# Kernel optimization log

Hardware: AMD Instinct MI355X
Metric: run time of the kernel (lower is better)

The kernel has to match this reference:

```python
import jax, jax.numpy as jnp
import numpy as np

N_NODES = 20000
NC = 16
NUM_BASIS = 5
MAX_CENTER = 3.5

# Real-basis Clebsch-Gordan tensors C[m, m_f, m_o] for the (l, l_f) -> l_o paths.
# Real l=1 basis ordered (m=-1,0,1) = (y,z,x); (y,z,x) is a cyclic permutation of
# (x,y,z) so the standard Levi-Civita gives the 1x1->1 coupling.
_C000 = np.ones((1, 1, 1), dtype=np.float32)
_C011 = np.eye(3, dtype=np.float32).reshape(1, 3, 3)
_C101 = np.eye(3, dtype=np.float32).reshape(3, 1, 3)
_C110 = (np.eye(3, dtype=np.float32) / np.sqrt(3.0)).reshape(3, 3, 1)
_eps = np.zeros((3, 3, 3), dtype=np.float32)
for (i, j, k) in [(0, 1, 2), (1, 2, 0), (2, 0, 1)]:
    _eps[i, j, k] = 1.0
    _eps[i, k, j] = -1.0
_C111 = (_eps / np.sqrt(2.0)).astype(np.float32)

Y00 = 0.28209479177387814  # 1 / (2 sqrt(pi))
Y1C = 0.4886025119029199   # sqrt(3 / (4 pi))


def _spherical_filter(edges, coeffs, l_f):
    """SphericalFilter.__call__: RBF radial part x solid harmonics. -> [E, n_c, 2l_f+1]."""
    centers = jnp.linspace(0.0, MAX_CENTER, NUM_BASIS)
    spread = (MAX_CENTER - 0.0) / NUM_BASIS  # (max - min) / num_basis = 0.7
    radius = jnp.linalg.norm(edges, ord=2, axis=-1)              # [E]
    rbfs = jnp.exp(-spread * (radius[:, None] - centers) ** 2)   # [E, num_basis]
    rad = rbfs @ coeffs.T                                        # [E, n_c]
    if l_f == 0:
        y = jnp.full(edges.shape[:-1] + (1,), Y00, dtype=edges.dtype)
    else:  # l_f == 1: solid harmonics r^1 * Y_1m, order (y, z, x)
        y = Y1C * edges[:, jnp.array([1, 2, 0])]
    y = jnp.nan_to_num(y)
    return rad[:, :, None] * y[:, None, :]


def _tp(nodes, filt, cg, w):
    """Depthwise CG tensor product: [E,c,m],[E,c,f],[m,f,o] -> w[c] * [E,c,o]."""
    out = jnp.einsum('ecm,ecf,mfo->eco', nodes, filt, jnp.asarray(cg))
    return w[None, :, None] * out


def setup_inputs() -> dict:
    key = jax.random.key(0)
    ks = jax.random.split(key, 16)
    E = 640000
    inp = {
        'coords': jax.random.normal(ks[0], (N_NODES, 3), dtype=jnp.float32),
        'nodes0': jax.random.normal(ks[1], (N_NODES, NC, 1), dtype=jnp.float32),
        'nodes1': jax.random.normal(ks[2], (N_NODES, NC, 3), dtype=jnp.float32),
        'edges': jax.random.normal(ks[3], (E, 3), dtype=jnp.float32),
        'senders': jax.random.randint(ks[4], (E,), 0, N_NODES, dtype=jnp.int32),
        'receivers': jax.random.randint(ks[5], (E,), 0, N_NODES, dtype=jnp.int32),
        'coeffs_00': jax.random.uniform(ks[6], (NC, NUM_BASIS), dtype=jnp.float32),
        'coeffs_01': jax.random.uniform(ks[7], (NC, NUM_BASIS), dtype=jnp.float32),
        'coeffs_10': jax.random.uniform(ks[8], (NC, NUM_BASIS), dtype=jnp.float32),
        'coeffs_11': jax.random.uniform(ks[9], (NC, NUM_BASIS), dtype=jnp.float32),
        'w_000': jax.random.normal(ks[10], (NC,), dtype=jnp.float32) + 1.0,
        'w_011': jax.random.normal(ks[11], (NC,), dtype=jnp.float32) + 1.0,
        'w_101': jax.random.normal(ks[12], (NC,), dtype=jnp.float32) + 1.0,
        'w_110': jax.random.normal(ks[13], (NC,), dtype=jnp.float32) + 1.0,
        'w_111': jax.random.normal(ks[14], (NC,), dtype=jnp.float32) + 1.0,
    }
    return inp


def reference(coords, nodes0, nodes1, edges, senders, receivers,
              coeffs_00, coeffs_01, coeffs_10, coeffs_11,
              w_000, w_011, w_101, w_110, w_111):
    # Gather sender node features once per l.
    n0s = nodes0[senders]  # [E, NC, 1]
    n1s = nodes1[senders]  # [E, NC, 3]

    # Filters (loop order: l=0 filters [l_f=0, l_f=1], then l=1 filters).
    f00 = _spherical_filter(edges, coeffs_00, 0)  # [E, NC, 1]
    f01 = _spherical_filter(edges, coeffs_01, 1)  # [E, NC, 3]
    f10 = _spherical_filter(edges, coeffs_10, 0)  # [E, NC, 1]
    f11 = _spherical_filter(edges, coeffs_11, 1)  # [E, NC, 3]

    # Tensor-product messages, concatenated per output degree along channels.
    # l_o = 0 paths: (l=0, l_f=0), (l=1, l_f=1)
    m0 = jnp.concatenate([
        _tp(n0s, f00, _C000, w_000),
        _tp(n1s, f11, _C110, w_110),
    ], axis=-2)  # [E, 2*NC, 1]
    # l_o = 1 paths: (0,1), (1,0), (1,1)
    m1 = jnp.concatenate([
        _tp(n0s, f01, _C011, w_011),
        _tp(n1s, f10, _C101, w_101),
        _tp(n1s, f11, _C111, w_111),
    ], axis=-2)  # [E, 3*NC, 3]

    new0 = jax.ops.segment_sum(m0, receivers, num_segments=N_NODES)
    new1 = jax.ops.segment_sum(m1, receivers, num_segments=N_NODES)
    return coords, new0, new1
```

## Files before the change

kernel.cpp:

```cpp
#include <hip/hip_runtime.h>

#define E_EDGES 640000
#define NN 20000
#define NC 16
#define PBIN 64

#define Y00F 0.28209479177387814f
#define Y1CF 0.4886025119029199f
#define RS3  0.5773502691896258f
#define RS2  0.7071067811865476f

typedef float nf4 __attribute__((ext_vector_type(4)));

struct Acc {
    float a000, a110;
    float a011x, a011y, a011z;
    float a101x, a101y, a101z;
    float a111x, a111y, a111z;
};

__device__ __forceinline__ void edge_body(const nf4 rec,
                                          const float* __restrict__ nodes0,
                                          const float* __restrict__ nodes1,
                                          const float k00[5], const float k01[5],
                                          const float k10[5], const float k11[5],
                                          int c, Acc& A) {
    int s = __float_as_int(rec.w);
    float r = sqrtf(rec.x * rec.x + rec.y * rec.y + rec.z * rec.z);
    float rbf[5];
#pragma unroll
    for (int b = 0; b < 5; b++) {
        float d = r - 0.875f * (float)b;
        rbf[b] = __expf(-0.7f * d * d);
    }
    float rad00 = 0.f, rad01 = 0.f, rad10 = 0.f, rad11 = 0.f;
#pragma unroll
    for (int b = 0; b < 5; b++) {
        rad00 = fmaf(rbf[b], k00[b], rad00);
        rad01 = fmaf(rbf[b], k01[b], rad01);
        rad10 = fmaf(rbf[b], k10[b], rad10);
        rad11 = fmaf(rbf[b], k11[b], rad11);
    }
    float n0 = nodes0[s * NC + c];
    const float* n1p = nodes1 + (s * NC + c) * 3;
    float n1a = n1p[0], n1b = n1p[1], n1c = n1p[2];
    float py = rec.y, pz = rec.z, px = rec.x;
    A.a000 = fmaf(n0, rad00, A.a000);
    A.a110 = fmaf(rad11, n1a * py + n1b * pz + n1c * px, A.a110);
    float kA = n0 * rad01;
    A.a011x = fmaf(kA, py, A.a011x);
    A.a011y = fmaf(kA, pz, A.a011y);
    A.a011z = fmaf(kA, px, A.a011z);
    A.a101x = fmaf(rad10, n1a, A.a101x);
    A.a101y = fmaf(rad10, n1b, A.a101y);
    A.a101z = fmaf(rad10, n1c, A.a101z);
    A.a111x = fmaf(rad11, n1b * px - n1c * pz, A.a111x);
    A.a111y = fmaf(rad11, n1c * py - n1a * px, A.a111y);
    A.a111z = fmaf(rad11, n1a * pz - n1b * py, A.a111z);
}


__global__ void init1_kernel(const float* __restrict__ coords,
                             float* __restrict__ out,
                             int* __restrict__ cnt,
                             int* __restrict__ ovf_count) {
    int i = blockIdx.x * blockDim.x + threadIdx.x;
    if (i < 3 * NN) out[i] = coords[i];
    if (i < NN) cnt[i] = 0;
    if (i == 0) *ovf_count = 0;
}

__global__ void bin_kernel(const float* __restrict__ edges,
                           const int* __restrict__ senders,
                           const int* __restrict__ receivers,
                           int* __restrict__ cnt,
                           nf4* __restrict__ bins,
                           int* __restrict__ ovf_count,
                           int* __restrict__ ovf_list) {
    int e = blockIdx.x * blockDim.x + threadIdx.x;
    if (e >= E_EDGES) return;
    float ex = edges[3 * e + 0];
    float ey = edges[3 * e + 1];
    float ez = edges[3 * e + 2];
    int s  = senders[e];
    int rc = receivers[e];
    int pos = atomicAdd(&cnt[rc], 1);
    if (pos < PBIN) {
        nf4 rec = {ex, ey, ez, __int_as_float(s)};
        bins[rc * PBIN + pos] = rec;
    } else {
        int k = atomicAdd(ovf_count, 1);
        if (k < 4096) ovf_list[k] = e;
    }
}

__global__ __launch_bounds__(256) void gather1_kernel(
    const nf4*    __restrict__ bins,
    const int*    __restrict__ cnt,
    const float*  __restrict__ nodes0,
    const float*  __restrict__ nodes1,
    const float*  __restrict__ c00, const float* __restrict__ c01,
    const float*  __restrict__ c10, const float* __restrict__ c11,
    const float*  __restrict__ w000, const float* __restrict__ w011,
    const float*  __restrict__ w101, const float* __restrict__ w110,
    const float*  __restrict__ w111,
    float* __restrict__ out0, float* __restrict__ out1)
{
    int gtid = blockIdx.x * blockDim.x + threadIdx.x;
    int node = gtid >> 6;
    int lane = threadIdx.x & 63;
    int c    = lane & 15;
    int j    = lane >> 4;
    if (node >= NN) return;

    float k00[5], k01[5], k10[5], k11[5];
#pragma unroll
    for (int b = 0; b < 5; b++) {
        k00[b] = c00[c * 5 + b];
        k01[b] = c01[c * 5 + b];
        k10[b] = c10[c * 5 + b];
        k11[b] = c11[c * 5 + b];
    }

    int n = cnt[node];
    n = (n < PBIN) ? n : PBIN;
    const nf4* base = bins + node * PBIN;

    Acc A = {};
    int i = j;
    for (; i + 4 < n; i += 8) {
        nf4 r0 = __builtin_nontemporal_load(&base[i]);
        nf4 r1 = __builtin_nontemporal_load(&base[i + 4]);
        edge_body(r0, nodes0, nodes1, k00, k01, k10, k11, c, A);
        edge_body(r1, nodes0, nodes1, k00, k01, k10, k11, c, A);
    }
    if (i < n) {
        nf4 r0 = __builtin_nontemporal_load(&base[i]);
        edge_body(r0, nodes0, nodes1, k00, k01, k10, k11, c, A);
    }

#define RED(v) v += __shfl_xor(v, 16, 64); v += __shfl_xor(v, 32, 64)
    RED(A.a000); RED(A.a110);
    RED(A.a011x); RED(A.a011y); RED(A.a011z);
    RED(A.a101x); RED(A.a101y); RED(A.a101z);
    RED(A.a111x); RED(A.a111y); RED(A.a111z);
#undef RED

    if (j == 0) {
        float s000 = w000[c] * Y00F;
        float s110 = w110[c] * RS3 * Y1CF;
        float s011 = w011[c] * Y1CF;
        float s101 = w101[c] * Y00F;
        float s111 = w111[c] * RS2 * Y1CF;

        out0[node * 32 + c]      = s000 * A.a000;
        out0[node * 32 + 16 + c] = s110 * A.a110;

        float* o1 = out1 + node * 144;
        o1[3 * c + 0] = s011 * A.a011x;
        o1[3 * c + 1] = s011 * A.a011y;
        o1[3 * c + 2] = s011 * A.a011z;
        o1[3 * (16 + c) + 0] = s101 * A.a101x;
        o1[3 * (16 + c) + 1] = s101 * A.a101y;
        o1[3 * (16 + c) + 2] = s101 * A.a101z;
        o1[3 * (32 + c) + 0] = s111 * A.a111x;
        o1[3 * (32 + c) + 1] = s111 * A.a111y;
        o1[3 * (32 + c) + 2] = s111 * A.a111z;
    }
}

__global__ void cleanup_kernel(
    const int* __restrict__ ovf_count, const int* __restrict__ ovf_list,
    const float* __restrict__ edges, const int* __restrict__ senders,
    const int* __restrict__ receivers,
    const float* __restrict__ nodes0, const float* __restrict__ nodes1,
    const float* __restrict__ c00, const float* __restrict__ c01,
    const float* __restrict__ c10, const float* __restrict__ c11,
    const float* __restrict__ w000, const float* __restrict__ w011,
    const float* __restrict__ w101, const float* __restrict__ w110,
    const float* __restrict__ w111,
    float* __restrict__ out0, float* __restrict__ out1)
{
    int nov = *ovf_count;
    if (nov > 4096) nov = 4096;
    for (int k = threadIdx.x; k < nov; k += blockDim.x) {
        int e = ovf_list[k];
        float ex = edges[3 * e + 0], ey = edges[3 * e + 1], ez = edges[3 * e + 2];
        float r = sqrtf(ex * ex + ey * ey + ez * ez);
        float rbf[5];
#pragma unroll
        for (int b = 0; b < 5; b++) {
            float d = r - 0.875f * (float)b;
            rbf[b] = __expf(-0.7f * d * d);
        }
        int s = senders[e], rc = receivers[e];
        const float* n0p = nodes0 + s * NC;
        const float* n1p = nodes1 + s * NC * 3;
        float* o0 = out0 + rc * 32;
        float* o1 = out1 + rc * 144;
        float pey = Y1CF * ey, pez = Y1CF * ez, pex = Y1CF * ex;
        for (int c = 0; c < NC; c++) {
            float rad00 = 0.f, rad01 = 0.f, rad10 = 0.f, rad11 = 0.f;
#pragma unroll
            for (int b = 0; b < 5; b++) {
                rad00 = fmaf(rbf[b], c00[c * 5 + b], rad00);
                rad01 = fmaf(rbf[b], c01[c * 5 + b], rad01);
                rad10 = fmaf(rbf[b], c10[c * 5 + b], rad10);
                rad11 = fmaf(rbf[b], c11[c * 5 + b], rad11);
            }
            float n0 = n0p[c];
            float n1a = n1p[3 * c + 0], n1b = n1p[3 * c + 1], n1c = n1p[3 * c + 2];
            float f11a = rad11 * pey, f11b = rad11 * pez, f11c = rad11 * pex;
            atomicAdd(&o0[c], w000[c] * n0 * rad00 * Y00F);
            atomicAdd(&o0[16 + c], w110[c] * RS3 * (n1a * f11a + n1b * f11b + n1c * f11c));
            float kA = w011[c] * n0 * rad01;
            atomicAdd(&o1[3 * c + 0], kA * pey);
            atomicAdd(&o1[3 * c + 1], kA * pez);
            atomicAdd(&o1[3 * c + 2], kA * pex);
            float kB = w101[c] * rad10 * Y00F;
            atomicAdd(&o1[3 * (16 + c) + 0], kB * n1a);
            atomicAdd(&o1[3 * (16 + c) + 1], kB * n1b);
            atomicAdd(&o1[3 * (16 + c) + 2], kB * n1c);
            float kC = w111[c] * RS2;
            atomicAdd(&o1[3 * (32 + c) + 0], kC * (n1b * f11c - n1c * f11b));
            atomicAdd(&o1[3 * (32 + c) + 1], kC * (n1c * f11a - n1a * f11c));
            atomicAdd(&o1[3 * (32 + c) + 2], kC * (n1a * f11b - n1b * f11a));
        }
    }
}

__global__ void init2_kernel(const float* __restrict__ coords,
                             float* __restrict__ out, int* __restrict__ hist) {
    int i = blockIdx.x * blockDim.x + threadIdx.x;
    if (i < 3 * NN) out[i] = coords[i];
    if (i < NN) hist[i] = 0;
}

__global__ void hist_kernel(const int* __restrict__ receivers,
                            int* __restrict__ hist) {
    int t = blockIdx.x * blockDim.x + threadIdx.x;
    if (t >= E_EDGES / 4) return;
    int4 r = *(const int4*)(receivers + 4 * t);
    atomicAdd(&hist[r.x], 1);
    atomicAdd(&hist[r.y], 1);
    atomicAdd(&hist[r.z], 1);
    atomicAdd(&hist[r.w], 1);
}

__global__ __launch_bounds__(1024) void scan1_kernel(const int* __restrict__ hist,
                                                     int* __restrict__ offs,
                                                     int* __restrict__ btot) {
    __shared__ int sh[1024];
    int t = threadIdx.x, b = blockIdx.x;
    int i = b * 1024 + t;
    int v = (i < NN) ? hist[i] : 0;
    sh[t] = v;
    __syncthreads();
    for (int off = 1; off < 1024; off <<= 1) {
        int x = (t >= off) ? sh[t - off] : 0;
        __syncthreads();
        sh[t] += x;
        __syncthreads();
    }
    int incl = sh[t];
    if (i < NN) offs[i] = incl - v;
    if (t == 1023) btot[b] = incl;
}

__global__ __launch_bounds__(1024) void scan2_kernel(int* __restrict__ offs,
                                                     int* __restrict__ cursor,
                                                     const int* __restrict__ btot,
                                                     int nblk) {
    __shared__ int pre[64];
    int t = threadIdx.x, b = blockIdx.x;
    if (t == 0) {
        int s = 0;
        for (int k = 0; k < nblk; k++) { pre[k] = s; s += btot[k]; }
    }
    __syncthreads();
    int i = b * 1024 + t;
    if (i < NN) {
        int o = offs[i] + pre[b];
        offs[i] = o;
        cursor[i] = o;
    }
    if (b == 0 && t == 0) offs[NN] = E_EDGES;
}

__global__ void scatter_kernel(const float* __restrict__ edges,
                               const int* __restrict__ senders,
                               const int* __restrict__ receivers,
                               int* __restrict__ cursor,
                               nf4* __restrict__ sorted) {
    int e = blockIdx.x * blockDim.x + threadIdx.x;
    if (e >= E_EDGES) return;
    float ex = edges[3 * e + 0];
    float ey = edges[3 * e + 1];
    float ez = edges[3 * e + 2];
    int s  = senders[e];
    int rc = receivers[e];
    int pos = atomicAdd(&cursor[rc], 1);
    nf4 rec = {ex, ey, ez, __int_as_float(s)};
    sorted[pos] = rec;
}

__global__ __launch_bounds__(256) void gather2_kernel(
    const nf4*    __restrict__ sorted,
    const int*    __restrict__ offs,
    const float*  __restrict__ nodes0,
    const float*  __restrict__ nodes1,
    const float*  __restrict__ c00, const float* __restrict__ c01,
    const float*  __restrict__ c10, const float* __restrict__ c11,
    const float*  __restrict__ w000, const float* __restrict__ w011,
    const float*  __restrict__ w101, const float* __restrict__ w110,
    const float*  __restrict__ w111,
    float* __restrict__ out0, float* __restrict__ out1)
{
    int gtid = blockIdx.x * blockDim.x + threadIdx.x;
    int node = gtid >> 6;
    int lane = threadIdx.x & 63;
    int c    = lane & 15;
    int j    = lane >> 4;
    if (node >= NN) return;

    float k00[5], k01[5], k10[5], k11[5];
#pragma unroll
    for (int b = 0; b < 5; b++) {
        k00[b] = c00[c * 5 + b];
        k01[b] = c01[c * 5 + b];
        k10[b] = c10[c * 5 + b];
        k11[b] = c11[c * 5 + b];
    }

    int start = offs[node];
    int end   = offs[node + 1];

    Acc A = {};
    int i = start + j;
    for (; i + 4 < end; i += 8) {
        nf4 r0 = __builtin_nontemporal_load(&sorted[i]);
        nf4 r1 = __builtin_nontemporal_load(&sorted[i + 4]);
        edge_body(r0, nodes0, nodes1, k00, k01, k10, k11, c, A);
        edge_body(r1, nodes0, nodes1, k00, k01, k10, k11, c, A);
    }
    if (i < end) {
        nf4 r0 = __builtin_nontemporal_load(&sorted[i]);
        edge_body(r0, nodes0, nodes1, k00, k01, k10, k11, c, A);
    }

#define RED(v) v += __shfl_xor(v, 16, 64); v += __shfl_xor(v, 32, 64)
    RED(A.a000); RED(A.a110);
    RED(A.a011x); RED(A.a011y); RED(A.a011z);
    RED(A.a101x); RED(A.a101y); RED(A.a101z);
    RED(A.a111x); RED(A.a111y); RED(A.a111z);
#undef RED

    if (j == 0) {
        float s000 = w000[c] * Y00F;
        float s110 = w110[c] * RS3 * Y1CF;
        float s011 = w011[c] * Y1CF;
        float s101 = w101[c] * Y00F;
        float s111 = w111[c] * RS2 * Y1CF;

        out0[node * 32 + c]      = s000 * A.a000;
        out0[node * 32 + 16 + c] = s110 * A.a110;

        float* o1 = out1 + node * 144;
        o1[3 * c + 0] = s011 * A.a011x;
        o1[3 * c + 1] = s011 * A.a011y;
        o1[3 * c + 2] = s011 * A.a011z;
        o1[3 * (16 + c) + 0] = s101 * A.a101x;
        o1[3 * (16 + c) + 1] = s101 * A.a101y;
        o1[3 * (16 + c) + 2] = s101 * A.a101z;
        o1[3 * (32 + c) + 0] = s111 * A.a111x;
        o1[3 * (32 + c) + 1] = s111 * A.a111y;
        o1[3 * (32 + c) + 2] = s111 * A.a111z;
    }
}

__global__ void init_out_fb(const float* __restrict__ coords,
                            float* __restrict__ out, int out_size) {
    int i = blockIdx.x * blockDim.x + threadIdx.x;
    if (i < 3 * NN) out[i] = coords[i];
    else if (i < out_size) out[i] = 0.0f;
}

__global__ __launch_bounds__(256) void tp_edges_fb(
    const float* __restrict__ edges, const int* __restrict__ senders,
    const int* __restrict__ receivers, const float* __restrict__ nodes0,
    const float* __restrict__ nodes1,
    const float* __restrict__ c00, const float* __restrict__ c01,
    const float* __restrict__ c10, const float* __restrict__ c11,
    const float* __restrict__ w000, const float* __restrict__ w011,
    const float* __restrict__ w101, const float* __restrict__ w110,
    const float* __restrict__ w111,
    float* __restrict__ out0, float* __restrict__ out1) {
    int e = blockIdx.x * blockDim.x + threadIdx.x;
    if (e >= E_EDGES) return;
    float ex = edges[3 * e + 0], ey = edges[3 * e + 1], ez = edges[3 * e + 2];
    float r = sqrtf(ex * ex + ey * ey + ez * ez);
    float rbf[5];
#pragma unroll
    for (int b = 0; b < 5; b++) {
        float d = r - 0.875f * (float)b;
        rbf[b] = __expf(-0.7f * d * d);
    }
    int s = senders[e], rc = receivers[e];
    const float* n0p = nodes0 + s * NC;
    const float* n1p = nodes1 + s * NC * 3;
    float* o0 = out0 + rc * 32;
    float* o1 = out1 + rc * 144;
    float pey = Y1CF * ey, pez = Y1CF * ez, pex = Y1CF * ex;
    for (int c = 0; c < NC; c++) {
        float rad00 = 0.f, rad01 = 0.f, rad10 = 0.f, rad11 = 0.f;
#pragma unroll
        for (int b = 0; b < 5; b++) {
            rad00 = fmaf(rbf[b], c00[c * 5 + b], rad00);
            rad01 = fmaf(rbf[b], c01[c * 5 + b], rad01);
            rad10 = fmaf(rbf[b], c10[c * 5 + b], rad10);
            rad11 = fmaf(rbf[b], c11[c * 5 + b], rad11);
        }
        float n0 = n0p[c];
        float n1a = n1p[3 * c + 0], n1b = n1p[3 * c + 1], n1c = n1p[3 * c + 2];
        float f11a = rad11 * pey, f11b = rad11 * pez, f11c = rad11 * pex;
        atomicAdd(&o0[c], w000[c] * n0 * rad00 * Y00F);
        atomicAdd(&o0[16 + c], w110[c] * RS3 * (n1a * f11a + n1b * f11b + n1c * f11c));
        float kA = w011[c] * n0 * rad01;
        atomicAdd(&o1[3 * c + 0], kA * pey);
        atomicAdd(&o1[3 * c + 1], kA * pez);
        atomicAdd(&o1[3 * c + 2], kA * pex);
        float kB = w101[c] * rad10 * Y00F;
        atomicAdd(&o1[3 * (16 + c) + 0], kB * n1a);
        atomicAdd(&o1[3 * (16 + c) + 1], kB * n1b);
        atomicAdd(&o1[3 * (16 + c) + 2], kB * n1c);
        float kC = w111[c] * RS2;
        atomicAdd(&o1[3 * (32 + c) + 0], kC * (n1b * f11c - n1c * f11b));
        atomicAdd(&o1[3 * (32 + c) + 1], kC * (n1c * f11a - n1a * f11c));
        atomicAdd(&o1[3 * (32 + c) + 2], kC * (n1a * f11b - n1b * f11a));
    }
}

extern "C" void kernel_launch(void* const* d_in, const int* in_sizes, int n_in,
                              void* d_out, int out_size, void* d_ws, size_t ws_size,
                              hipStream_t stream) {
    const float* coords    = (const float*)d_in[0];
    const float* nodes0    = (const float*)d_in[1];
    const float* nodes1    = (const float*)d_in[2];
    const float* edges     = (const float*)d_in[3];
    const int*   senders   = (const int*)  d_in[4];
    const int*   receivers = (const int*)  d_in[5];
    const float* c00       = (const float*)d_in[6];
    const float* c01       = (const float*)d_in[7];
    const float* c10       = (const float*)d_in[8];
    const float* c11       = (const float*)d_in[9];
    const float* w000      = (const float*)d_in[10];
    const float* w011      = (const float*)d_in[11];
    const float* w101      = (const float*)d_in[12];
    const float* w110      = (const float*)d_in[13];
    const float* w111      = (const float*)d_in[14];

    float* out  = (float*)d_out;
    float* out0 = out + 3 * NN;
    float* out1 = out + 3 * NN + NN * 2 * NC;

    size_t bins_bytes = (size_t)NN * PBIN * 16;
    size_t need1 = bins_bytes + (size_t)(NN + 1 + 4096) * 4;
    size_t sorted_bytes = (size_t)E_EDGES * 16;
    size_t need2 = sorted_bytes + (size_t)(3 * NN + 1 + 64) * 4;

    if (ws_size >= need1) {
        nf4* bins      = (nf4*)d_ws;
        int* cnt       = (int*)((char*)d_ws + bins_bytes);
        int* ovf_count = cnt + NN;
        int* ovf_list  = ovf_count + 1;

        init1_kernel<<<(3 * NN + 255) / 256, 256, 0, stream>>>(coords, out, cnt, ovf_count);
        bin_kernel<<<(E_EDGES + 255) / 256, 256, 0, stream>>>(
            edges, senders, receivers, cnt, bins, ovf_count, ovf_list);
        gather1_kernel<<<(NN * 64 + 255) / 256, 256, 0, stream>>>(
            bins, cnt, nodes0, nodes1,
            c00, c01, c10, c11, w000, w011, w101, w110, w111, out0, out1);
        cleanup_kernel<<<1, 256, 0, stream>>>(
            ovf_count, ovf_list, edges, senders, receivers, nodes0, nodes1,
            c00, c01, c10, c11, w000, w011, w101, w110, w111, out0, out1);
    } else if (ws_size >= need2) {
        nf4* sorted = (nf4*)d_ws;
        int* offs   = (int*)((char*)d_ws + sorted_bytes);
        int* cursor = offs + (NN + 1);
        int* hist   = cursor + NN;
        int* btot   = hist + NN;
        const int NBLK = (NN + 1023) / 1024;

        init2_kernel<<<(3 * NN + 255) / 256, 256, 0, stream>>>(coords, out, hist);
        hist_kernel<<<(E_EDGES / 4 + 255) / 256, 256, 0, stream>>>(receivers, hist);
        scan1_kernel<<<NBLK, 1024, 0, stream>>>(hist, offs, btot);
        scan2_kernel<<<NBLK, 1024, 0, stream>>>(offs, cursor, btot, NBLK);
        scatter_kernel<<<(E_EDGES + 255) / 256, 256, 0, stream>>>(
            edges, senders, receivers, cursor, sorted);
        gather2_kernel<<<(NN * 64 + 255) / 256, 256, 0, stream>>>(
            sorted, offs, nodes0, nodes1,
            c00, c01, c10, c11, w000, w011, w101, w110, w111, out0, out1);
    } else {
        init_out_fb<<<(out_size + 255) / 256, 256, 0, stream>>>(coords, out, out_size);
        tp_edges_fb<<<(E_EDGES + 255) / 256, 256, 0, stream>>>(
            edges, senders, receivers, nodes0, nodes1,
            c00, c01, c10, c11, w000, w011, w101, w110, w111, out0, out1);
    }
}
```

Before: 171.2 us.

## Precompute per-edge RBF factors in binning and use Horner polynomial in gather

The binning kernel now computes, once per edge, the Gaussian factor exp(-0.7 r^2) and t = exp(1.225 r), plus the pre-scaled spherical harmonic components. It stores these in a 32-byte record instead of a 16-byte one. The gather kernel, which runs once per (edge, channel) lane, rebuilds the four radial mixes as A * polynomial(t) using Horner with coefficients scaled by constant factors, so it no longer needs five exps per edge per lane. This trades doubled bin storage and read bandwidth for fewer transcendental operations. The sorted-scatter fallback path is also removed, and expanding exp(1.225r) powers could lose precision for large r.

```diff
diff --git a/kernel.cpp b/kernel.cpp
--- a/kernel.cpp
+++ b/kernel.cpp
@@ -18,46 +18,6 @@
     float a101x, a101y, a101z;
     float a111x, a111y, a111z;
 };
-
-__device__ __forceinline__ void edge_body(const nf4 rec,
-                                          const float* __restrict__ nodes0,
-                                          const float* __restrict__ nodes1,
-                                          const float k00[5], const float k01[5],
-                                          const float k10[5], const float k11[5],
-                                          int c, Acc& A) {
-    int s = __float_as_int(rec.w);
-    float r = sqrtf(rec.x * rec.x + rec.y * rec.y + rec.z * rec.z);
-    float rbf[5];
-#pragma unroll
-    for (int b = 0; b < 5; b++) {
-        float d = r - 0.875f * (float)b;
-        rbf[b] = __expf(-0.7f * d * d);
-    }
-    float rad00 = 0.f, rad01 = 0.f, rad10 = 0.f, rad11 = 0.f;
-#pragma unroll
-    for (int b = 0; b < 5; b++) {
-        rad00 = fmaf(rbf[b], k00[b], rad00);
-        rad01 = fmaf(rbf[b], k01[b], rad01);
-        rad10 = fmaf(rbf[b], k10[b], rad10);
-        rad11 = fmaf(rbf[b], k11[b], rad11);
-    }
-    float n0 = nodes0[s * NC + c];
-    const float* n1p = nodes1 + (s * NC + c) * 3;
-    float n1a = n1p[0], n1b = n1p[1], n1c = n1p[2];
-    float py = rec.y, pz = rec.z, px = rec.x;
-    A.a000 = fmaf(n0, rad00, A.a000);
-    A.a110 = fmaf(rad11, n1a * py + n1b * pz + n1c * px, A.a110);
-    float kA = n0 * rad01;
-    A.a011x = fmaf(kA, py, A.a011x);
-    A.a011y = fmaf(kA, pz, A.a011y);
-    A.a011z = fmaf(kA, px, A.a011z);
-    A.a101x = fmaf(rad10, n1a, A.a101x);
-    A.a101y = fmaf(rad10, n1b, A.a101y);
-    A.a101z = fmaf(rad10, n1c, A.a101z);
-    A.a111x = fmaf(rad11, n1b * px - n1c * pz, A.a111x);
-    A.a111y = fmaf(rad11, n1c * py - n1a * px, A.a111y);
-    A.a111z = fmaf(rad11, n1a * pz - n1b * py, A.a111z);
-}
 
 
 __global__ void init1_kernel(const float* __restrict__ coords,
@@ -86,8 +46,15 @@
     int rc = receivers[e];
     int pos = atomicAdd(&cnt[rc], 1);
     if (pos < PBIN) {
-        nf4 rec = {ex, ey, ez, __int_as_float(s)};
-        bins[rc * PBIN + pos] = rec;
+        float r2 = ex * ex + ey * ey + ez * ez;
+        float r  = sqrtf(r2);
+        float A  = __expf(-0.7f * r2);
+        float t  = __expf(1.225f * r);
+        nf4 r0 = {Y1CF * ey, Y1CF * ez, Y1CF * ex, __int_as_float(s)};
+        nf4 r1 = {A, t, 0.0f, 0.0f};
+        nf4* p = bins + 2 * ((size_t)rc * PBIN + pos);
+        p[0] = r0;
+        p[1] = r1;
     } else {
         int k = atomicAdd(ovf_count, 1);
         if (k < 4096) ovf_list[k] = e;
@@ -113,31 +80,65 @@
     int j    = lane >> 4;
     if (node >= NN) return;
 
+    const float KB[5] = {1.0f, 0.58512723f, 0.11721218f, 0.00803909f, 1.8876652e-4f};
     float k00[5], k01[5], k10[5], k11[5];
 #pragma unroll
     for (int b = 0; b < 5; b++) {
-        k00[b] = c00[c * 5 + b];
-        k01[b] = c01[c * 5 + b];
-        k10[b] = c10[c * 5 + b];
-        k11[b] = c11[c * 5 + b];
+        k00[b] = c00[c * 5 + b] * KB[b];
+        k01[b] = c01[c * 5 + b] * KB[b];
+        k10[b] = c10[c * 5 + b] * KB[b];
+        k11[b] = c11[c * 5 + b] * KB[b];
     }
 
     int n = cnt[node];
     n = (n < PBIN) ? n : PBIN;
-    const nf4* base = bins + node * PBIN;
+    const nf4* base = bins + 2 * (size_t)node * PBIN;
 
     Acc A = {};
+
+#define HORNER(k, t) fmaf((t), fmaf((t), fmaf((t), fmaf((t), k[4], k[3]), k[2]), k[1]), k[0])
+#define BODY(r0, r1)                                                       \
+    {                                                                      \
+        int s = __float_as_int(r0.w);                                      \
+        float Af = r1.x, tf = r1.y;                                        \
+        float rad00 = Af * HORNER(k00, tf);                                \
+        float rad01 = Af * HORNER(k01, tf);                                \
+        float rad10 = Af * HORNER(k10, tf);                                \
+        float rad11 = Af * HORNER(k11, tf);                                \
+        float n0 = nodes0[s * NC + c];                                     \
+        const float* n1p = nodes1 + (s * NC + c) * 3;                      \
+        float n1a = n1p[0], n1b = n1p[1], n1c = n1p[2];                    \
+        float py = r0.x, pz = r0.y, px = r0.z;                             \
+        A.a000 = fmaf(n0, rad00, A.a000);                                  \
+        A.a110 = fmaf(rad11, n1a * py + n1b * pz + n1c * px, A.a110);      \
+        float kA = n0 * rad01;                                             \
+        A.a011x = fmaf(kA, py, A.a011x);                                   \
+        A.a011y = fmaf(kA, pz, A.a011y);                                   \
+        A.a011z = fmaf(kA, px, A.a011z);                                   \
+        A.a101x = fmaf(rad10, n1a, A.a101x);                               \
+        A.a101y = fmaf(rad10, n1b, A.a101y);                               \
+        A.a101z = fmaf(rad10, n1c, A.a101z);                               \
+        A.a111x = fmaf(rad11, n1b * px - n1c * pz, A.a111x);               \
+        A.a111y = fmaf(rad11, n1c * py - n1a * px, A.a111y);               \
+        A.a111z = fmaf(rad11, n1a * pz - n1b * py, A.a111z);               \
+    }
+
     int i = j;
     for (; i + 4 < n; i += 8) {
-        nf4 r0 = __builtin_nontemporal_load(&base[i]);
-        nf4 r1 = __builtin_nontemporal_load(&base[i + 4]);
-        edge_body(r0, nodes0, nodes1, k00, k01, k10, k11, c, A);
-        edge_body(r1, nodes0, nodes1, k00, k01, k10, k11, c, A);
+        nf4 a0 = __builtin_nontemporal_load(&base[2 * i]);
+        nf4 a1 = __builtin_nontemporal_load(&base[2 * i + 1]);
+        nf4 b0 = __builtin_nontemporal_load(&base[2 * (i + 4)]);
+        nf4 b1 = __builtin_nontemporal_load(&base[2 * (i + 4) + 1]);
+        BODY(a0, a1);
+        BODY(b0, b1);
     }
     if (i < n) {
-        nf4 r0 = __builtin_nontemporal_load(&base[i]);
-        edge_body(r0, nodes0, nodes1, k00, k01, k10, k11, c, A);
-    }
+        nf4 a0 = __builtin_nontemporal_load(&base[2 * i]);
+        nf4 a1 = __builtin_nontemporal_load(&base[2 * i + 1]);
+        BODY(a0, a1);
+    }
+#undef BODY
+#undef HORNER
 
 #define RED(v) v += __shfl_xor(v, 16, 64); v += __shfl_xor(v, 32, 64)
     RED(A.a000); RED(A.a110);
@@ -148,10 +149,10 @@
 
     if (j == 0) {
         float s000 = w000[c] * Y00F;
-        float s110 = w110[c] * RS3 * Y1CF;
-        float s011 = w011[c] * Y1CF;
+        float s110 = w110[c] * RS3;
+        float s011 = w011[c];
         float s101 = w101[c] * Y00F;
-        float s111 = w111[c] * RS2 * Y1CF;
+        float s111 = w111[c] * RS2;
 
         out0[node * 32 + c]      = s000 * A.a000;
         out0[node * 32 + 16 + c] = s110 * A.a110;
@@ -229,155 +230,6 @@
     }
 }
 
-__global__ void init2_kernel(const float* __restrict__ coords,
-                             float* __restrict__ out, int* __restrict__ hist) {
-    int i = blockIdx.x * blockDim.x + threadIdx.x;
-    if (i < 3 * NN) out[i] = coords[i];
-    if (i < NN) hist[i] = 0;
-}
-
-__global__ void hist_kernel(const int* __restrict__ receivers,
-                            int* __restrict__ hist) {
-    int t = blockIdx.x * blockDim.x + threadIdx.x;
-    if (t >= E_EDGES / 4) return;
-    int4 r = *(const int4*)(receivers + 4 * t);
-    atomicAdd(&hist[r.x], 1);
-    atomicAdd(&hist[r.y], 1);
-    atomicAdd(&hist[r.z], 1);
-    atomicAdd(&hist[r.w], 1);
-}
-
-__global__ __launch_bounds__(1024) void scan1_kernel(const int* __restrict__ hist,
-                                                     int* __restrict__ offs,
-                                                     int* __restrict__ btot) {
-    __shared__ int sh[1024];
-    int t = threadIdx.x, b = blockIdx.x;
-    int i = b * 1024 + t;
-    int v = (i < NN) ? hist[i] : 0;
-    sh[t] = v;
-    __syncthreads();
-    for (int off = 1; off < 1024; off <<= 1) {
-        int x = (t >= off) ? sh[t - off] : 0;
-        __syncthreads();
-        sh[t] += x;
-        __syncthreads();
-    }
-    int incl = sh[t];
-    if (i < NN) offs[i] = incl - v;
-    if (t == 1023) btot[b] = incl;
-}
-
-__global__ __launch_bounds__(1024) void scan2_kernel(int* __restrict__ offs,
-                                                     int* __restrict__ cursor,
-                                                     const int* __restrict__ btot,
-                                                     int nblk) {
-    __shared__ int pre[64];
-    int t = threadIdx.x, b = blockIdx.x;
-    if (t == 0) {
-        int s = 0;
-        for (int k = 0; k < nblk; k++) { pre[k] = s; s += btot[k]; }
-    }
-    __syncthreads();
-    int i = b * 1024 + t;
-    if (i < NN) {
-        int o = offs[i] + pre[b];
-        offs[i] = o;
-        cursor[i] = o;
-    }
-    if (b == 0 && t == 0) offs[NN] = E_EDGES;
-}
-
-__global__ void scatter_kernel(const float* __restrict__ edges,
-                               const int* __restrict__ senders,
-                               const int* __restrict__ receivers,
-                               int* __restrict__ cursor,
-                               nf4* __restrict__ sorted) {
-    int e = blockIdx.x * blockDim.x + threadIdx.x;
-    if (e >= E_EDGES) return;
-    float ex = edges[3 * e + 0];
-    float ey = edges[3 * e + 1];
-    float ez = edges[3 * e + 2];
-    int s  = senders[e];
-    int rc = receivers[e];
-    int pos = atomicAdd(&cursor[rc], 1);
-    nf4 rec = {ex, ey, ez, __int_as_float(s)};
-    sorted[pos] = rec;
-}
-
-__global__ __launch_bounds__(256) void gather2_kernel(
-    const nf4*    __restrict__ sorted,
-    const int*    __restrict__ offs,
-    const float*  __restrict__ nodes0,
-    const float*  __restrict__ nodes1,
-    const float*  __restrict__ c00, const float* __restrict__ c01,
-    const float*  __restrict__ c10, const float* __restrict__ c11,
-    const float*  __restrict__ w000, const float* __restrict__ w011,
-    const float*  __restrict__ w101, const float* __restrict__ w110,
-    const float*  __restrict__ w111,
-    float* __restrict__ out0, float* __restrict__ out1)
-{
-    int gtid = blockIdx.x * blockDim.x + threadIdx.x;
-    int node = gtid >> 6;
-    int lane = threadIdx.x & 63;
-    int c    = lane & 15;
-    int j    = lane >> 4;
-    if (node >= NN) return;
-
-    float k00[5], k01[5], k10[5], k11[5];
-#pragma unroll
-    for (int b = 0; b < 5; b++) {
-        k00[b] = c00[c * 5 + b];
-        k01[b] = c01[c * 5 + b];
-        k10[b] = c10[c * 5 + b];
-        k11[b] = c11[c * 5 + b];
-    }
-
-    int start = offs[node];
-    int end   = offs[node + 1];
-
-    Acc A = {};
-    int i = start + j;
-    for (; i + 4 < end; i += 8) {
-        nf4 r0 = __builtin_nontemporal_load(&sorted[i]);
-        nf4 r1 = __builtin_nontemporal_load(&sorted[i + 4]);
-        edge_body(r0, nodes0, nodes1, k00, k01, k10, k11, c, A);
-        edge_body(r1, nodes0, nodes1, k00, k01, k10, k11, c, A);
-    }
-    if (i < end) {
-        nf4 r0 = __builtin_nontemporal_load(&sorted[i]);
-        edge_body(r0, nodes0, nodes1, k00, k01, k10, k11, c, A);
-    }
-
-#define RED(v) v += __shfl_xor(v, 16, 64); v += __shfl_xor(v, 32, 64)
-    RED(A.a000); RED(A.a110);
-    RED(A.a011x); RED(A.a011y); RED(A.a011z);
-    RED(A.a101x); RED(A.a101y); RED(A.a101z);
-    RED(A.a111x); RED(A.a111y); RED(A.a111z);
-#undef RED
-
-    if (j == 0) {
-        float s000 = w000[c] * Y00F;
-        float s110 = w110[c] * RS3 * Y1CF;
-        float s011 = w011[c] * Y1CF;
-        float s101 = w101[c] * Y00F;
-        float s111 = w111[c] * RS2 * Y1CF;
-
-        out0[node * 32 + c]      = s000 * A.a000;
-        out0[node * 32 + 16 + c] = s110 * A.a110;
-
-        float* o1 = out1 + node * 144;
-        o1[3 * c + 0] = s011 * A.a011x;
-        o1[3 * c + 1] = s011 * A.a011y;
-        o1[3 * c + 2] = s011 * A.a011z;
-        o1[3 * (16 + c) + 0] = s101 * A.a101x;
-        o1[3 * (16 + c) + 1] = s101 * A.a101y;
-        o1[3 * (16 + c) + 2] = s101 * A.a101z;
-        o1[3 * (32 + c) + 0] = s111 * A.a111x;
-        o1[3 * (32 + c) + 1] = s111 * A.a111y;
-        o1[3 * (32 + c) + 2] = s111 * A.a111z;
-    }
-}
-
 __global__ void init_out_fb(const float* __restrict__ coords,
                             float* __restrict__ out, int out_size) {
     int i = blockIdx.x * blockDim.x + threadIdx.x;
@@ -463,10 +315,8 @@
     float* out0 = out + 3 * NN;
     float* out1 = out + 3 * NN + NN * 2 * NC;
 
-    size_t bins_bytes = (size_t)NN * PBIN * 16;
+    size_t bins_bytes = (size_t)NN * PBIN * 32;
     size_t need1 = bins_bytes + (size_t)(NN + 1 + 4096) * 4;
-    size_t sorted_bytes = (size_t)E_EDGES * 16;
-    size_t need2 = sorted_bytes + (size_t)(3 * NN + 1 + 64) * 4;
 
     if (ws_size >= need1) {
         nf4* bins      = (nf4*)d_ws;
@@ -483,23 +333,6 @@
         cleanup_kernel<<<1, 256, 0, stream>>>(
             ovf_count, ovf_list, edges, senders, receivers, nodes0, nodes1,
             c00, c01, c10, c11, w000, w011, w101, w110, w111, out0, out1);
-    } else if (ws_size >= need2) {
-        nf4* sorted = (nf4*)d_ws;
-        int* offs   = (int*)((char*)d_ws + sorted_bytes);
-        int* cursor = offs + (NN + 1);
-        int* hist   = cursor + NN;
-        int* btot   = hist + NN;
-        const int NBLK = (NN + 1023) / 1024;
-
-        init2_kernel<<<(3 * NN + 255) / 256, 256, 0, stream>>>(coords, out, hist);
-        hist_kernel<<<(E_EDGES / 4 + 255) / 256, 256, 0, stream>>>(receivers, hist);
-        scan1_kernel<<<NBLK, 1024, 0, stream>>>(hist, offs, btot);
-        scan2_kernel<<<NBLK, 1024, 0, stream>>>(offs, cursor, btot, NBLK);
-        scatter_kernel<<<(E_EDGES + 255) / 256, 256, 0, stream>>>(
-            edges, senders, receivers, cursor, sorted);
-        gather2_kernel<<<(NN * 64 + 255) / 256, 256, 0, stream>>>(
-            sorted, offs, nodes0, nodes1,
-            c00, c01, c10, c11, w000, w011, w101, w110, w111, out0, out1);
     } else {
         init_out_fb<<<(out_size + 255) / 256, 256, 0, stream>>>(coords, out, out_size);
         tp_edges_fb<<<(E_EDGES + 255) / 256, 256, 0, stream>>>(
```

Result: slower. 179.8 us (+5.0%).
